# Kernel tuning notes

Measured on AMD Instinct MI355X. Metric: run time of the kernel, lower is better.

Reference implementation:

```python
import jax, jax.numpy as jnp
import numpy as np

H = 32          # query heads
D = 128         # head_dim
THETA = 10000.0
NEG = -1e30


def _rope_cos_sin(positions, d):
    half = d // 2
    inv_freq = 1.0 / (THETA ** (jnp.arange(0, d, 2, dtype=jnp.float32) / d))  # [half]
    ang = positions.astype(jnp.float32)[:, None] * inv_freq[None, :]          # [B, half]
    return jnp.cos(ang), jnp.sin(ang)


def _apply_rope(x, cos, sin):
    # neox-style rotary on last dim; cos/sin broadcast over leading dims
    half = x.shape[-1] // 2
    x1, x2 = x[..., :half], x[..., half:]
    return jnp.concatenate([x1 * cos - x2 * sin, x2 * cos + x1 * sin], axis=-1)


def setup_inputs() -> dict:
    key = jax.random.key(0)
    ks = jax.random.split(key, 8)
    B, hidden = 64, 4096
    num_blocks, block_size, max_blocks = 16384, 16, 256
    hidden_states = jax.random.normal(ks[0], (B, hidden), dtype=jnp.float32)
    wqkv = jax.random.normal(ks[1], (hidden, (H + 2) * D), dtype=jnp.float32) * 0.02
    wdense = jax.random.normal(ks[2], (hidden, hidden), dtype=jnp.float32) * 0.02
    k_cache = jax.random.normal(ks[3], (num_blocks, block_size, D), dtype=jnp.float32)
    v_cache = jax.random.normal(ks[4], (num_blocks, block_size, D), dtype=jnp.float32)
    # each sequence owns a distinct set of 256 blocks
    block_tables = jnp.arange(B * max_blocks, dtype=jnp.int64).reshape(B, max_blocks)
    context_lens = jax.random.randint(ks[5], (B,), 1, max_blocks * block_size + 1).astype(jnp.int64)
    positions = context_lens - 1  # position of the new (current) token
    return {
        "hidden_states": hidden_states, "wqkv": wqkv, "wdense": wdense,
        "k_cache": k_cache, "v_cache": v_cache,
        "positions": positions, "block_tables": block_tables,
        "context_lens": context_lens,
    }


def reference(hidden_states, wqkv, wdense, k_cache, v_cache,
              positions, block_tables, context_lens):
    B = hidden_states.shape[0]
    block_size = k_cache.shape[1]
    scale = 1.0 / np.sqrt(D).astype(np.float32)

    # fused QKV projection (bias=False in Falcon-7B config)
    qkv = hidden_states @ wqkv                                  # [B,(H+2)*D]
    q = qkv[:, : H * D].reshape(B, H, D)
    k = qkv[:, H * D : (H + 1) * D]                             # [B,D]  (MQA, 1 kv head)
    v = qkv[:, (H + 1) * D :]                                   # [B,D]

    # rotary embedding on q and k at the current positions
    cos, sin = _rope_cos_sin(positions, D)                      # [B,D/2]
    q = _apply_rope(q, cos[:, None, :], sin[:, None, :])
    k = _apply_rope(k, cos, sin)

    # write the new token's k/v into the paged cache (scatter)
    rows = jnp.arange(B)
    blk = block_tables[rows, positions // block_size]           # [B]
    off = positions % block_size
    k_cache = k_cache.at[blk, off].set(k)
    v_cache = v_cache.at[blk, off].set(v)

    # paged gather: assemble each sequence's KV from its block table
    keys = k_cache[block_tables].reshape(B, -1, D)              # [B,L,D]
    vals = v_cache[block_tables].reshape(B, -1, D)
    L = keys.shape[1]

    scores = jnp.einsum('bhd,bld->bhl', q, keys) * scale        # [B,H,L]
    valid = jnp.arange(L)[None, :] < context_lens[:, None]      # [B,L]
    scores = jnp.where(valid[:, None, :], scores, NEG)
    probs = jax.nn.softmax(scores, axis=-1)
    attn = jnp.einsum('bhl,bld->bhd', probs, vals).reshape(B, H * D)

    return attn @ wdense                                        # [B,hidden]
```

## Files before the change

### kernel.cpp

```cpp
#include <hip/hip_runtime.h>
#include <hip/hip_bf16.h>
#include <cmath>

#define NHEADS 32
#define DIM 128
#define SPLITS 16
#define TILE 32
#define KSPLIT 8
#define QKV_N 4352
#define HID 4096

typedef __attribute__((ext_vector_type(4))) float f32x4;
typedef __attribute__((ext_vector_type(8))) short short8i;
typedef __attribute__((ext_vector_type(4))) short short4i;

__device__ __forceinline__ unsigned short f2bf(float x) {
  __hip_bfloat16 h = __float2bfloat16(x);
  return *reinterpret_cast<unsigned short*>(&h);
}
__device__ __forceinline__ unsigned int pk2bf(float lo, float hi) {
  return (unsigned)f2bf(lo) | ((unsigned)f2bf(hi) << 16);
}

__device__ __forceinline__ f32x4 mfma16bf16(short4i a, short4i b, f32x4 c) {
#if __has_builtin(__builtin_amdgcn_mfma_f32_16x16x16bf16_1k)
  return __builtin_amdgcn_mfma_f32_16x16x16bf16_1k(a, b, c, 0, 0, 0);
#else
  asm volatile("v_mfma_f32_16x16x16_bf16 %0, %1, %2, %0"
               : "+v"(c) : "v"(a), "v"(b));
  return c;
#endif
}

__global__ __launch_bounds__(256, 4) void gemm64_mfma(
    const float* __restrict__ A, const float* __restrict__ W,
    float* __restrict__ P, int N, int K)
{
  __shared__ unsigned short Ab[64][40];
  __shared__ unsigned short Wt[64][40];
  const int t = threadIdx.x;
  const int w = t >> 6, lane = t & 63;
  const int l4 = lane >> 4, l16 = lane & 15;
  const int n0 = blockIdx.x * 64;
  const int KS = K / KSPLIT;
  const int kbase = blockIdx.y * KS;

  const int ar = t >> 2, akq = t & 3;
  const int bn = t & 63, bkq = t >> 6;

  f32x4 acc[4];
#pragma unroll
  for (int i = 0; i < 4; ++i) acc[i] = (f32x4){0.f, 0.f, 0.f, 0.f};

  float4 a0, a1;
  float bw[8];

#define GLOAD(KC)                                                          \
  {                                                                        \
    const float* ap = A + (size_t)ar * K + kbase + (KC) + akq * 8;         \
    a0 = *(const float4*)ap;                                               \
    a1 = *(const float4*)(ap + 4);                                         \
    const float* wp = W + (size_t)(kbase + (KC) + bkq * 8) * N + n0 + bn;  \
    _Pragma("unroll")                                                      \
    for (int j = 0; j < 8; ++j) bw[j] = wp[(size_t)j * N];                 \
  }

#define SWRITE                                                             \
  {                                                                        \
    unsigned int ua[4] = {pk2bf(a0.x, a0.y), pk2bf(a0.z, a0.w),            \
                          pk2bf(a1.x, a1.y), pk2bf(a1.z, a1.w)};           \
    *(float4*)&Ab[ar][akq * 8] = *(float4*)ua;                             \
    unsigned int ub[4] = {pk2bf(bw[0], bw[1]), pk2bf(bw[2], bw[3]),        \
                          pk2bf(bw[4], bw[5]), pk2bf(bw[6], bw[7])};       \
    *(float4*)&Wt[bn][bkq * 8] = *(float4*)ub;                             \
  }

  GLOAD(0);
  SWRITE;
  __syncthreads();

  for (int kc = 0; kc < KS; kc += 32) {
    const bool pre = (kc + 32 < KS);
    if (pre) GLOAD(kc + 32);

    const short8i af = *(const short8i*)&Ab[w * 16 + l16][l4 * 8];
#pragma unroll
    for (int nt = 0; nt < 4; ++nt) {
      const short8i bf = *(const short8i*)&Wt[nt * 16 + l16][l4 * 8];
      acc[nt] = __builtin_amdgcn_mfma_f32_16x16x32_bf16(af, bf, acc[nt], 0, 0, 0);
    }

    __syncthreads();
    if (pre) {
      SWRITE;
      __syncthreads();
    }
  }

  float* base = P + (size_t)blockIdx.y * 64 * N + n0;
#pragma unroll
  for (int nt = 0; nt < 4; ++nt)
#pragma unroll
    for (int r = 0; r < 4; ++r)
      base[(size_t)(w * 16 + l4 * 4 + r) * N + nt * 16 + l16] = acc[nt][r];
#undef GLOAD
#undef SWRITE
}

__global__ __launch_bounds__(256) void reduce_parts(
    const float* __restrict__ P, float* __restrict__ C, int total)
{
  const int i = (blockIdx.x * 256 + threadIdx.x) * 4;
  if (i >= total) return;
  float4 s = *(const float4*)(P + i);
#pragma unroll
  for (int k = 1; k < KSPLIT; ++k) {
    const float4 v = *(const float4*)(P + (size_t)k * total + i);
    s.x += v.x; s.y += v.y; s.z += v.z; s.w += v.w;
  }
  *(float4*)(C + i) = s;
}

__global__ __launch_bounds__(256) void reduce_rope(
    const float* __restrict__ P, float* __restrict__ qkv,
    const int* __restrict__ positions)
{
  const int id = blockIdx.x * 256 + threadIdx.x;
  const int b = id / 560;
  const int w = id - b * 560;
  const int total = 64 * QKV_N;
  const size_t rbase = (size_t)b * QKV_N;

  if (w < 528) {
    const int r = w >> 4;
    const int g = w & 15;
    const int base = (r < 32) ? r * DIM : HID;
    const int c1 = base + g * 4;
    const int c2 = c1 + 64;
    float4 s1 = *(const float4*)(P + rbase + c1);
    float4 s2 = *(const float4*)(P + rbase + c2);
#pragma unroll
    for (int k = 1; k < KSPLIT; ++k) {
      const float4 v1 = *(const float4*)(P + (size_t)k * total + rbase + c1);
      const float4 v2 = *(const float4*)(P + (size_t)k * total + rbase + c2);
      s1.x += v1.x; s1.y += v1.y; s1.z += v1.z; s1.w += v1.w;
      s2.x += v2.x; s2.y += v2.y; s2.z += v2.z; s2.w += v2.w;
    }
    const float pos = (float)positions[b];
    float o1[4], o2[4];
    const float sv1[4] = {s1.x, s1.y, s1.z, s1.w};
    const float sv2[4] = {s2.x, s2.y, s2.z, s2.w};
#pragma unroll
    for (int j = 0; j < 4; ++j) {
      const int d = g * 4 + j;
      const float ex = (float)d * (1.0f / 64.0f);
      const float inv = 1.0f / powf(10000.0f, ex);
      const float ang = pos * inv;
      const float c = cosf(ang), sn = sinf(ang);
      o1[j] = sv1[j] * c - sv2[j] * sn;
      o2[j] = sv2[j] * c + sv1[j] * sn;
    }
    *(float4*)(qkv + rbase + c1) = make_float4(o1[0], o1[1], o1[2], o1[3]);
    *(float4*)(qkv + rbase + c2) = make_float4(o2[0], o2[1], o2[2], o2[3]);
  } else {
    const int c = HID + DIM + (w - 528) * 4;
    float4 s = *(const float4*)(P + rbase + c);
#pragma unroll
    for (int k = 1; k < KSPLIT; ++k) {
      const float4 v = *(const float4*)(P + (size_t)k * total + rbase + c);
      s.x += v.x; s.y += v.y; s.z += v.z; s.w += v.w;
    }
    *(float4*)(qkv + rbase + c) = s;
  }
}

__global__ __launch_bounds__(256, 4) void attn_kernel(
    const float* __restrict__ qkv,
    const float* __restrict__ k_cache, const float* __restrict__ v_cache,
    const int* __restrict__ block_tables, const int* __restrict__ context_lens,
    float* __restrict__ pl, float* __restrict__ pacc)
{
  const int b = blockIdx.x, s = blockIdx.y;
  const int t = threadIdx.x;
  const int w = t >> 6, lane = t & 63;
  const int hq = w >> 1, pq = w & 1;
  const int l4 = lane >> 4, l16 = lane & 15;
  const int ctx = context_lens[b];
  const int pos = ctx - 1;
  const int chunk = (ctx + SPLITS - 1) / SPLITS;
  const int start = s * chunk;
  const int end = min(start + chunk, ctx);
  const int nt = (end > start) ? ((end - start + TILE - 1) / TILE) : 0;

  __shared__ unsigned short KbU[32 * 128];
  __shared__ unsigned short VtU[128 * 34];
  __shared__ float red[2][64][36];
  __shared__ int bt_lds[24];

  const float* qbase = qkv + (size_t)b * QKV_N;
  const int bt0 = start >> 4;
  if (t < 24) {
    const int idx = bt0 + t;
    bt_lds[t] = (idx < 256) ? block_tables[b * 256 + idx] : 0;
  }

  const float scale = 0.08838834764831845f;
  short8i qf[4];
  {
    const float* qp0 = qbase + (hq * 16 + l16) * DIM + l4 * 8;
#pragma unroll
    for (int ks = 0; ks < 4; ++ks) {
      const float4 a = *(const float4*)(qp0 + ks * 32);
      const float4 c = *(const float4*)(qp0 + ks * 32 + 4);
      union { unsigned int u[4]; short8i v; } qc;
      qc.u[0] = pk2bf(a.x * scale, a.y * scale);
      qc.u[1] = pk2bf(a.z * scale, a.w * scale);
      qc.u[2] = pk2bf(c.x * scale, c.y * scale);
      qc.u[3] = pk2bf(c.z * scale, c.w * scale);
      qf[ks] = qc.v;
    }
  }

  f32x4 o2[8];
#pragma unroll
  for (int i = 0; i < 8; ++i) o2[i] = (f32x4){0.f, 0.f, 0.f, 0.f};
  float lh = 0.f;

  float4 kreg[4], vreg[4];
  const int tk_sub = t >> 5;
  const int tk_col = t & 31;

#define LOADREGS(T0)                                                     \
  {                                                                      \
    _Pragma("unroll")                                                    \
    for (int j = 0; j < 4; ++j) {                                        \
      int gp_ = (T0) + j * 8 + tk_sub;                                   \
      if (gp_ > pos) gp_ = pos;                                          \
      const float* kp;                                                   \
      if (gp_ == pos) kp = qbase + HID;                                  \
      else {                                                             \
        const int blk = bt_lds[(gp_ >> 4) - bt0];                        \
        kp = k_cache + ((size_t)blk * 16 + (gp_ & 15)) * DIM;            \
      }                                                                  \
      kreg[j] = *(const float4*)(kp + tk_col * 4);                       \
    }                                                                    \
    int gv = (T0) + tk_col;                                              \
    if (gv > pos) gv = pos;                                              \
    const float* vp;                                                     \
    if (gv == pos) vp = qbase + HID + DIM;                               \
    else {                                                               \
      const int blk = bt_lds[(gv >> 4) - bt0];                           \
      vp = v_cache + ((size_t)blk * 16 + (gv & 15)) * DIM;               \
    }                                                                    \
    _Pragma("unroll")                                                    \
    for (int j = 0; j < 4; ++j)                                          \
      vreg[j] = *(const float4*)(vp + tk_sub * 16 + j * 4);              \
  }

#define WRITE_TILE                                                                     \
  {                                                                                    \
    _Pragma("unroll")                                                                  \
    for (int j = 0; j < 4; ++j) {                                                      \
      const int pl_ = j * 8 + tk_sub;                                                  \
      const int up = (tk_col >> 1) ^ (pl_ & 15);                                       \
      unsigned int lo = pk2bf(kreg[j].x, kreg[j].y);                                   \
      unsigned int hi = pk2bf(kreg[j].z, kreg[j].w);                                   \
      unsigned int* dst = (unsigned int*)&KbU[pl_ * 128 + up * 8 + (tk_col & 1) * 4];  \
      dst[0] = lo; dst[1] = hi;                                                        \
    }                                                                                  \
    _Pragma("unroll")                                                                  \
    for (int j = 0; j < 4; ++j) {                                                      \
      const int od0 = tk_sub * 16 + j * 4;                                             \
      VtU[(od0 + 0) * 34 + tk_col] = f2bf(vreg[j].x);                                  \
      VtU[(od0 + 1) * 34 + tk_col] = f2bf(vreg[j].y);                                  \
      VtU[(od0 + 2) * 34 + tk_col] = f2bf(vreg[j].z);                                  \
      VtU[(od0 + 3) * 34 + tk_col] = f2bf(vreg[j].w);                                  \
    }                                                                                  \
  }

  if (nt > 0) {
    __syncthreads();
    LOADREGS(start);
    WRITE_TILE;
    __syncthreads();

    for (int it = 0; it < nt; ++it) {
      const int t0 = start + it * TILE;
      const bool pre = (it + 1 < nt);
      if (pre) LOADREGS(t0 + TILE);

      f32x4 accs = {0.f, 0.f, 0.f, 0.f};
      const int rowK = pq * 16 + l16;
#pragma unroll
      for (int ks = 0; ks < 4; ++ks) {
        const int up = (l4 + ks * 4) ^ l16;
        const short8i kf = *(const short8i*)&KbU[rowK * 128 + up * 8];
        accs = __builtin_amdgcn_mfma_f32_16x16x32_bf16(kf, qf[ks], accs, 0, 0, 0);
      }

      const int pb_ = t0 + pq * 16 + l4 * 4;
      const float p0 = (pb_ + 0 < end) ? __expf(accs[0]) : 0.f;
      const float p1 = (pb_ + 1 < end) ? __expf(accs[1]) : 0.f;
      const float p2 = (pb_ + 2 < end) ? __expf(accs[2]) : 0.f;
      const float p3 = (pb_ + 3 < end) ? __expf(accs[3]) : 0.f;
      lh += (p0 + p1) + (p2 + p3);
      union { unsigned int u[2]; short4i v; } pc;
      pc.u[0] = pk2bf(p0, p1);
      pc.u[1] = pk2bf(p2, p3);
      const short4i pf = pc.v;

      const int vb = pq * 16 + l4 * 4;
#pragma unroll
      for (int ob = 0; ob < 8; ++ob) {
        const int rowV = ob * 16 + l16;
        union { unsigned int u[2]; short4i v; } vc;
        vc.u[0] = *(const unsigned int*)&VtU[rowV * 34 + vb];
        vc.u[1] = *(const unsigned int*)&VtU[rowV * 34 + vb + 2];
        o2[ob] = mfma16bf16(pf, vc.v, o2[ob]);
      }

      if (pre) {
        __syncthreads();
        WRITE_TILE;
        __syncthreads();
      }
    }
  }

  float lhr = lh;
  lhr += __shfl_xor(lhr, 16);
  lhr += __shfl_xor(lhr, 32);

  if (pq == 1) {
#pragma unroll
    for (int ob = 0; ob < 8; ++ob) *(f32x4*)&red[hq][lane][ob * 4] = o2[ob];
    red[hq][lane][32] = lhr;
  }
  __syncthreads();
  if (pq == 0) {
#pragma unroll
    for (int ob = 0; ob < 8; ++ob) {
      const f32x4 r4 = *(const f32x4*)&red[hq][lane][ob * 4];
      o2[ob] += r4;
    }
    lhr += red[hq][lane][32];
    const size_t sbase = (size_t)(b * SPLITS + s) * NHEADS + hq * 16;
#pragma unroll
    for (int ob = 0; ob < 8; ++ob) {
      pacc[(sbase + l4 * 4 + 0) * DIM + ob * 16 + l16] = o2[ob][0];
      pacc[(sbase + l4 * 4 + 1) * DIM + ob * 16 + l16] = o2[ob][1];
      pacc[(sbase + l4 * 4 + 2) * DIM + ob * 16 + l16] = o2[ob][2];
      pacc[(sbase + l4 * 4 + 3) * DIM + ob * 16 + l16] = o2[ob][3];
    }
    if (lane < 16) pl[sbase + lane] = lhr;
  }
#undef LOADREGS
#undef WRITE_TILE
}

__global__ __launch_bounds__(128) void combine_kernel(
    const float* __restrict__ pl, const float* __restrict__ pacc,
    float* __restrict__ attn)
{
  const int bh = blockIdx.x;
  const int b = bh >> 5, h = bh & 31;
  const int d = threadIdx.x;
  float L = 0.f, o = 0.f;
#pragma unroll
  for (int s = 0; s < SPLITS; ++s) {
    const size_t idx = (size_t)(b * SPLITS + s) * NHEADS + h;
    L += pl[idx];
    o += pacc[idx * DIM + d];
  }
  attn[(size_t)b * HID + h * DIM + d] = o / L;
}

extern "C" void kernel_launch(void* const* d_in, const int* in_sizes, int n_in,
                              void* d_out, int out_size, void* d_ws, size_t ws_size,
                              hipStream_t stream) {
  const float* hidden   = (const float*)d_in[0];
  const float* wqkv     = (const float*)d_in[1];
  const float* wdense   = (const float*)d_in[2];
  const float* k_cache  = (const float*)d_in[3];
  const float* v_cache  = (const float*)d_in[4];
  const int* positions    = (const int*)d_in[5];
  const int* block_tables = (const int*)d_in[6];
  const int* context_lens = (const int*)d_in[7];
  float* out = (float*)d_out;

  float* qkv  = (float*)d_ws;
  float* attn = qkv + 64 * QKV_N;
  float* un   = attn + 64 * HID;
  float* gp   = un;
  float* pacc = un;
  float* pl   = pacc + (size_t)64 * SPLITS * NHEADS * DIM;

  gemm64_mfma<<<dim3(QKV_N / 64, KSPLIT), 256, 0, stream>>>(hidden, wqkv, gp, QKV_N, HID);
  reduce_rope<<<140, 256, 0, stream>>>(gp, qkv, positions);
  attn_kernel<<<dim3(64, SPLITS), 256, 0, stream>>>(qkv, k_cache, v_cache,
                                                    block_tables, context_lens, pl, pacc);
  combine_kernel<<<64 * NHEADS, 128, 0, stream>>>(pl, pacc, attn);
  gemm64_mfma<<<dim3(HID / 64, KSPLIT), 256, 0, stream>>>(attn, wdense, gp, HID, HID);
  reduce_parts<<<(64 * HID) / 1024, 256, 0, stream>>>(gp, out, 64 * HID);
}
```

Before: 96.26 us.

## Vectorize V tile loads/stores and write per-half partials in bf16 to combine

V loads now fetch two positions per thread with 8 contiguous dims, so V can be packed into LDS as 32-bit bf16 pairs instead of scattered 16-bit stores. The in-block LDS reduction between the two position-halves is removed, along with its barrier. Each half now writes its own partial accumulator in bf16, and the combine kernel sums twice as many splits. This cuts LDS traffic and a sync at the cost of more, lower-precision partial data that combine has to read.

```diff
diff --git a/kernel.cpp b/kernel.cpp
--- a/kernel.cpp
+++ b/kernel.cpp
@@ -20,6 +20,10 @@
 }
 __device__ __forceinline__ unsigned int pk2bf(float lo, float hi) {
   return (unsigned)f2bf(lo) | ((unsigned)f2bf(hi) << 16);
+}
+__device__ __forceinline__ float bf2f(unsigned short u) {
+  unsigned int b = ((unsigned int)u) << 16;
+  return __uint_as_float(b);
 }
 
 __device__ __forceinline__ f32x4 mfma16bf16(short4i a, short4i b, f32x4 c) {
@@ -178,7 +182,7 @@
     const float* __restrict__ qkv,
     const float* __restrict__ k_cache, const float* __restrict__ v_cache,
     const int* __restrict__ block_tables, const int* __restrict__ context_lens,
-    float* __restrict__ pl, float* __restrict__ pacc)
+    float* __restrict__ pl, unsigned short* __restrict__ pacc)
 {
   const int b = blockIdx.x, s = blockIdx.y;
   const int t = threadIdx.x;
@@ -194,7 +198,6 @@
 
   __shared__ unsigned short KbU[32 * 128];
   __shared__ unsigned short VtU[128 * 34];
-  __shared__ float red[2][64][36];
   __shared__ int bt_lds[24];
 
   const float* qbase = qkv + (size_t)b * QKV_N;
@@ -229,6 +232,8 @@
   float4 kreg[4], vreg[4];
   const int tk_sub = t >> 5;
   const int tk_col = t & 31;
+  const int vp2 = tk_sub + 8 * (tk_col >> 4);
+  const int vd0 = (tk_col & 15) * 8;
 
 #define LOADREGS(T0)                                                     \
   {                                                                      \
@@ -244,17 +249,19 @@
       }                                                                  \
       kreg[j] = *(const float4*)(kp + tk_col * 4);                       \
     }                                                                    \
-    int gv = (T0) + tk_col;                                              \
-    if (gv > pos) gv = pos;                                              \
-    const float* vp;                                                     \
-    if (gv == pos) vp = qbase + HID + DIM;                               \
-    else {                                                               \
-      const int blk = bt_lds[(gv >> 4) - bt0];                           \
-      vp = v_cache + ((size_t)blk * 16 + (gv & 15)) * DIM;               \
+    _Pragma("unroll")                                                    \
+    for (int j = 0; j < 2; ++j) {                                        \
+      int gv_ = (T0) + vp2 * 2 + j;                                      \
+      if (gv_ > pos) gv_ = pos;                                          \
+      const float* vp;                                                   \
+      if (gv_ == pos) vp = qbase + HID + DIM;                            \
+      else {                                                             \
+        const int blk = bt_lds[(gv_ >> 4) - bt0];                        \
+        vp = v_cache + ((size_t)blk * 16 + (gv_ & 15)) * DIM;            \
+      }                                                                  \
+      vreg[j * 2 + 0] = *(const float4*)(vp + vd0);                      \
+      vreg[j * 2 + 1] = *(const float4*)(vp + vd0 + 4);                  \
     }                                                                    \
-    _Pragma("unroll")                                                    \
-    for (int j = 0; j < 4; ++j)                                          \
-      vreg[j] = *(const float4*)(vp + tk_sub * 16 + j * 4);              \
   }
 
 #define WRITE_TILE                                                                     \
@@ -263,18 +270,20 @@
     for (int j = 0; j < 4; ++j) {                                                      \
       const int pl_ = j * 8 + tk_sub;                                                  \
       const int up = (tk_col >> 1) ^ (pl_ & 15);                                       \
-      unsigned int lo = pk2bf(kreg[j].x, kreg[j].y);                                   \
-      unsigned int hi = pk2bf(kreg[j].z, kreg[j].w);                                   \
-      unsigned int* dst = (unsigned int*)&KbU[pl_ * 128 + up * 8 + (tk_col & 1) * 4];  \
-      dst[0] = lo; dst[1] = hi;                                                        \
+      unsigned int* kd = (unsigned int*)&KbU[pl_ * 128 + up * 8 + (tk_col & 1) * 4];   \
+      kd[0] = pk2bf(kreg[j].x, kreg[j].y);                                             \
+      kd[1] = pk2bf(kreg[j].z, kreg[j].w);                                             \
     }                                                                                  \
-    _Pragma("unroll")                                                                  \
-    for (int j = 0; j < 4; ++j) {                                                      \
-      const int od0 = tk_sub * 16 + j * 4;                                             \
-      VtU[(od0 + 0) * 34 + tk_col] = f2bf(vreg[j].x);                                  \
-      VtU[(od0 + 1) * 34 + tk_col] = f2bf(vreg[j].y);                                  \
-      VtU[(od0 + 2) * 34 + tk_col] = f2bf(vreg[j].z);                                  \
-      VtU[(od0 + 3) * 34 + tk_col] = f2bf(vreg[j].w);                                  \
+    {                                                                                  \
+      const int pc_ = vp2 * 2;                                                         \
+      *(unsigned int*)&VtU[(vd0 + 0) * 34 + pc_] = pk2bf(vreg[0].x, vreg[2].x);        \
+      *(unsigned int*)&VtU[(vd0 + 1) * 34 + pc_] = pk2bf(vreg[0].y, vreg[2].y);        \
+      *(unsigned int*)&VtU[(vd0 + 2) * 34 + pc_] = pk2bf(vreg[0].z, vreg[2].z);        \
+      *(unsigned int*)&VtU[(vd0 + 3) * 34 + pc_] = pk2bf(vreg[0].w, vreg[2].w);        \
+      *(unsigned int*)&VtU[(vd0 + 4) * 34 + pc_] = pk2bf(vreg[1].x, vreg[3].x);        \
+      *(unsigned int*)&VtU[(vd0 + 5) * 34 + pc_] = pk2bf(vreg[1].y, vreg[3].y);        \
+      *(unsigned int*)&VtU[(vd0 + 6) * 34 + pc_] = pk2bf(vreg[1].z, vreg[3].z);        \
+      *(unsigned int*)&VtU[(vd0 + 7) * 34 + pc_] = pk2bf(vreg[1].w, vreg[3].w);        \
     }                                                                                  \
   }
 
@@ -331,46 +340,32 @@
   lhr += __shfl_xor(lhr, 16);
   lhr += __shfl_xor(lhr, 32);
 
-  if (pq == 1) {
-#pragma unroll
-    for (int ob = 0; ob < 8; ++ob) *(f32x4*)&red[hq][lane][ob * 4] = o2[ob];
-    red[hq][lane][32] = lhr;
-  }
-  __syncthreads();
-  if (pq == 0) {
-#pragma unroll
-    for (int ob = 0; ob < 8; ++ob) {
-      const f32x4 r4 = *(const f32x4*)&red[hq][lane][ob * 4];
-      o2[ob] += r4;
-    }
-    lhr += red[hq][lane][32];
-    const size_t sbase = (size_t)(b * SPLITS + s) * NHEADS + hq * 16;
-#pragma unroll
-    for (int ob = 0; ob < 8; ++ob) {
-      pacc[(sbase + l4 * 4 + 0) * DIM + ob * 16 + l16] = o2[ob][0];
-      pacc[(sbase + l4 * 4 + 1) * DIM + ob * 16 + l16] = o2[ob][1];
-      pacc[(sbase + l4 * 4 + 2) * DIM + ob * 16 + l16] = o2[ob][2];
-      pacc[(sbase + l4 * 4 + 3) * DIM + ob * 16 + l16] = o2[ob][3];
-    }
-    if (lane < 16) pl[sbase + lane] = lhr;
-  }
+  const size_t slot = ((size_t)(b * SPLITS + s) * 2 + pq) * NHEADS + hq * 16;
+#pragma unroll
+  for (int ob = 0; ob < 8; ++ob) {
+    pacc[(slot + l4 * 4 + 0) * DIM + ob * 16 + l16] = f2bf(o2[ob][0]);
+    pacc[(slot + l4 * 4 + 1) * DIM + ob * 16 + l16] = f2bf(o2[ob][1]);
+    pacc[(slot + l4 * 4 + 2) * DIM + ob * 16 + l16] = f2bf(o2[ob][2]);
+    pacc[(slot + l4 * 4 + 3) * DIM + ob * 16 + l16] = f2bf(o2[ob][3]);
+  }
+  if (lane < 16) pl[slot + lane] = lhr;
 #undef LOADREGS
 #undef WRITE_TILE
 }
 
 __global__ __launch_bounds__(128) void combine_kernel(
-    const float* __restrict__ pl, const float* __restrict__ pacc,
+    const float* __restrict__ pl, const unsigned short* __restrict__ pacc,
     float* __restrict__ attn)
 {
   const int bh = blockIdx.x;
   const int b = bh >> 5, h = bh & 31;
   const int d = threadIdx.x;
   float L = 0.f, o = 0.f;
-#pragma unroll
-  for (int s = 0; s < SPLITS; ++s) {
-    const size_t idx = (size_t)(b * SPLITS + s) * NHEADS + h;
+#pragma unroll 4
+  for (int j = 0; j < SPLITS * 2; ++j) {
+    const size_t idx = ((size_t)b * SPLITS * 2 + j) * NHEADS + h;
     L += pl[idx];
-    o += pacc[idx * DIM + d];
+    o += bf2f(pacc[idx * DIM + d]);
   }
   attn[(size_t)b * HID + h * DIM + d] = o / L;
 }
@@ -392,8 +387,8 @@
   float* attn = qkv + 64 * QKV_N;
   float* un   = attn + 64 * HID;
   float* gp   = un;
-  float* pacc = un;
-  float* pl   = pacc + (size_t)64 * SPLITS * NHEADS * DIM;
+  unsigned short* pacc = (unsigned short*)un;
+  float* pl   = un + (size_t)64 * SPLITS * 2 * NHEADS * DIM / 2;
 
   gemm64_mfma<<<dim3(QKV_N / 64, KSPLIT), 256, 0, stream>>>(hidden, wqkv, gp, QKV_N, HID);
   reduce_rope<<<140, 256, 0, stream>>>(gp, qkv, positions);
```

Result: faster. 92.46 us, median of 2 (-4.0%).
